# Kernel optimization log

Hardware: AMD Instinct MI355X
Metric: run time of the kernel (lower is better)

Reference implementation:

```python
import jax, jax.numpy as jnp
import numpy as np

N_EMBD = 1024
NUM_HEADS = 16
HEAD_SIZE = N_EMBD // NUM_HEADS
B, T = 2, 2048


def setup_inputs() -> dict:
    key = jax.random.key(0)
    k1, k2, k3, k4 = jax.random.split(key, 4)
    x = jax.random.normal(k1, (B, T, N_EMBD), dtype=jnp.float32)
    # torch nn.Linear weight is [out,in]; we store transposed [in,out] for x @ W
    w_qkv = jax.random.normal(k2, (N_EMBD, 3 * N_EMBD), dtype=jnp.float32) * (N_EMBD ** -0.5)
    w_proj = jax.random.normal(k3, (N_EMBD, N_EMBD), dtype=jnp.float32) * (N_EMBD ** -0.5)
    b_proj = jax.random.normal(k4, (N_EMBD,), dtype=jnp.float32) * 0.01
    return {"x": x, "w_qkv": w_qkv, "w_proj": w_proj, "b_proj": b_proj}


def reference(x, w_qkv, w_proj, b_proj):
    Bm, Tm, C = x.shape
    H, D = NUM_HEADS, HEAD_SIZE
    qkv = x @ w_qkv  # [B,T,3C]
    # einops 'b t (h d three) -> three b h t d': 'three' is the innermost factor
    qkv = qkv.reshape(Bm, Tm, H, D, 3)
    q = qkv[..., 0].transpose(0, 2, 1, 3)  # [B,H,T,D]
    k = qkv[..., 1].transpose(0, 2, 1, 3)
    v = qkv[..., 2].transpose(0, 2, 1, 3)
    scale = D ** -0.5
    attn = jnp.einsum('bhqd,bhkd->bhqk', q, k) * scale  # [B,H,T,T]
    causal_mask = jnp.triu(jnp.ones((Tm, Tm), dtype=bool), k=1)
    attn = jnp.where(causal_mask, -jnp.inf, attn)
    attn = jax.nn.softmax(attn, axis=-1)
    out = jnp.einsum('bhqk,bhkd->bhqd', attn, v)  # [B,H,T,D]
    out = out.transpose(0, 2, 1, 3).reshape(Bm, Tm, C)  # b h t d -> b t (h d)
    out = out @ w_proj + b_proj
    return out
```

## Files before the change

### kernel.cpp

```cpp
#include <hip/hip_runtime.h>
#include <hip/hip_bf16.h>
#include <math.h>

typedef __bf16 bf16x8 __attribute__((ext_vector_type(8)));
typedef __bf16 bf16x4 __attribute__((ext_vector_type(4)));
typedef float f32x4 __attribute__((ext_vector_type(4)));

#define MFMA16(A, B, C) __builtin_amdgcn_mfma_f32_16x16x32_bf16(A, B, C, 0, 0, 0)

__device__ __forceinline__ void cp16(void* lds_base, const void* g) {
  __builtin_amdgcn_global_load_lds(
      (const __attribute__((address_space(1))) void*)g,
      (__attribute__((address_space(3))) void*)lds_base, 16, 0, 0);
}

static constexpr int Bc   = 2;
static constexpr int Tc   = 2048;
static constexpr int Cc   = 1024;
static constexpr int Hc   = 16;
static constexpr int Dc   = 64;
static constexpr int Mrows = Bc * Tc;
static constexpr int N3    = 3 * Cc;

__global__ __launch_bounds__(256) void convert_x(
    const float* __restrict__ src, __bf16* __restrict__ dst, int n) {
  const int i0 = (blockIdx.x * 256 + threadIdx.x) * 8;
  if (i0 >= n) return;
  f32x4 a = *(const f32x4*)(src + i0);
  f32x4 b = *(const f32x4*)(src + i0 + 4);
  bf16x8 v;
#pragma unroll
  for (int j = 0; j < 4; ++j) { v[j] = (__bf16)a[j]; v[4 + j] = (__bf16)b[j]; }
  *(bf16x8*)(dst + i0) = v;
}

__global__ __launch_bounds__(256) void transpose_weights(
    const float* __restrict__ wqkv, const float* __restrict__ wproj,
    __bf16* __restrict__ dqkv, __bf16* __restrict__ dproj) {
  __shared__ __bf16 tile[32][33];
  const bool isproj = blockIdx.x >= 96;
  const float* src = isproj ? wproj : wqkv;
  __bf16* dst = isproj ? dproj : dqkv;
  const int N = isproj ? Cc : N3;
  const int K = Cc;
  const int n0 = (isproj ? (blockIdx.x - 96) : blockIdx.x) * 32;
  const int k0 = blockIdx.y * 32;
  const int x = threadIdx.x & 31;
  const int y = threadIdx.x >> 5;
  {
    int n = n0 + x;
    int col = n;
    if (!isproj) {
      int three = n >> 10, rem = n & 1023;
      int h = rem >> 6, d = rem & 63;
      col = h * 192 + d * 3 + three;
    }
#pragma unroll
    for (int r = 0; r < 4; ++r) {
      int k = k0 + y + r * 8;
      tile[y + r * 8][x] = (__bf16)src[(size_t)k * N + col];
    }
  }
  __syncthreads();
#pragma unroll
  for (int r = 0; r < 4; ++r) {
    int n = n0 + y + r * 8;
    dst[(size_t)n * K + k0 + x] = tile[x][y + r * 8];
  }
}

__global__ __launch_bounds__(256) void v_transpose(
    const __bf16* __restrict__ qkvp, __bf16* __restrict__ vt) {
  __shared__ __bf16 tile[32][33];
  const int t0 = blockIdx.x * 32;
  const int d0 = blockIdx.y * 32;
  const int bh = blockIdx.z;
  const int b = bh >> 4, h = bh & 15;
  const int x = threadIdx.x & 31;
  const int y = threadIdx.x >> 5;
#pragma unroll
  for (int r = 0; r < 4; ++r) {
    int t = t0 + y + r * 8;
    tile[y + r * 8][x] =
        qkvp[(size_t)(b * Tc + t) * N3 + 2 * Cc + h * 64 + d0 + x];
  }
  __syncthreads();
#pragma unroll
  for (int r = 0; r < 4; ++r) {
    int d = d0 + y + r * 8;
    vt[((size_t)bh * 64 + d) * Tc + t0 + x] = tile[x][y + r * 8];
  }
}

template <bool F32OUT>
__global__ __launch_bounds__(256) void gemm_nt(
    const __bf16* __restrict__ A, const __bf16* __restrict__ Bt,
    void* __restrict__ Cmat, const float* __restrict__ bias,
    int M, int N, int K, int ldc) {
  __shared__ __align__(16) __bf16 As[128 * 64];
  __shared__ __align__(16) __bf16 Bs[128 * 64];
  const int n0 = blockIdx.x * 128, m0 = blockIdx.y * 128;
  const int tid = threadIdx.x;
  const int wave = tid >> 6, lane = tid & 63;
  const int quad = lane >> 4, l16 = lane & 15;
  const int wm = (wave >> 1) * 64, wn = (wave & 1) * 64;
  const int srow = lane >> 3;
  const int scol = (((lane & 7) ^ (srow & 7))) * 8;

  f32x4 acc[4][4] = {};

  for (int k0 = 0; k0 < K; k0 += 64) {
    __syncthreads();
#pragma unroll
    for (int c = 0; c < 4; ++c) {
      int rowblk = c * 4 + wave;
      int row = rowblk * 8 + srow;
      cp16(&As[rowblk * 512], A + (size_t)(m0 + row) * K + k0 + scol);
      cp16(&Bs[rowblk * 512], Bt + (size_t)(n0 + row) * K + k0 + scol);
    }
    __syncthreads();
#pragma unroll
    for (int kk = 0; kk < 64; kk += 32) {
      bf16x8 af[4], bfr[4];
#pragma unroll
      for (int i = 0; i < 4; ++i) {
        int chunk = (((kk >> 3) + quad) ^ (l16 & 7)) * 8;
        af[i]  = *(const bf16x8*)(&As[(wm + i * 16 + l16) * 64 + chunk]);
        bfr[i] = *(const bf16x8*)(&Bs[(wn + i * 16 + l16) * 64 + chunk]);
      }
#pragma unroll
      for (int mi = 0; mi < 4; ++mi)
#pragma unroll
        for (int ni = 0; ni < 4; ++ni)
          acc[mi][ni] = MFMA16(af[mi], bfr[ni], acc[mi][ni]);
    }
  }

#pragma unroll
  for (int ni = 0; ni < 4; ++ni) {
    int col = n0 + wn + ni * 16 + l16;
    float bv = bias ? bias[col] : 0.0f;
#pragma unroll
    for (int mi = 0; mi < 4; ++mi)
#pragma unroll
      for (int r = 0; r < 4; ++r) {
        int row = m0 + wm + mi * 16 + quad * 4 + r;
        float v = acc[mi][ni][r] + bv;
        if (F32OUT)
          ((float*)Cmat)[(size_t)row * ldc + col] = v;
        else
          ((__bf16*)Cmat)[(size_t)row * ldc + col] = (__bf16)v;
      }
  }
}

#define LOG2E 1.44269504088896340736f
#define C2SC  (0.125f * LOG2E)
#define SH2   (16.0f * LOG2E)
static constexpr int LPK = 72;
static constexpr int LPV = 136;
static constexpr int TB  = 128;

__global__ __launch_bounds__(256) void attn_kernel(
    const __bf16* __restrict__ qkv,
    const __bf16* __restrict__ vt,
    __bf16* __restrict__ obuf) {
  __shared__ __align__(16) __bf16 Ks[TB * LPK];
  __shared__ __align__(16) __bf16 Vs[64 * LPV];
  __shared__ __align__(16) __bf16 plds[4][2][16 * LPK];

  const int bh = blockIdx.x;
  const int torder = blockIdx.y;
  const int qt = (torder < 8) ? torder : (23 - torder);
  const int q0 = qt * 128;
  const int b = bh >> 4, hh = bh & 15;
  const int tid = threadIdx.x;
  const int wave = tid >> 6, lane = tid & 63;
  const int quad = lane >> 4, l16 = lane & 15;
  const int qb = q0 + wave * 32;
  const int kblocks = q0 + 128;

  const __bf16* qbase = qkv + (size_t)(b * Tc) * N3 + hh * 64;
  const __bf16* kbase = qbase + Cc;
  const __bf16* vtb = vt + (size_t)bh * 64 * Tc;

  const int krow = tid >> 1;
  const int kcol = (tid & 1) * 32;
  const int vrow = tid >> 2;
  const int vcol = (tid & 3) * 32;

  bf16x8 bQ[2][2];
#pragma unroll
  for (int hf = 0; hf < 2; ++hf) {
    const __bf16* qr = qbase + (size_t)(qb + hf * 16 + l16) * N3;
    bQ[hf][0] = *(const bf16x8*)(qr + quad * 8);
    bQ[hf][1] = *(const bf16x8*)(qr + 32 + quad * 8);
  }

  f32x4 accO[2][4] = {};
  float l_part[2] = {0.0f, 0.0f};

  bf16x8 kp[4], vp[4];
  {
    const __bf16* kr = kbase + (size_t)krow * N3 + kcol;
    const __bf16* vr = vtb + (size_t)vrow * Tc + vcol;
#pragma unroll
    for (int j = 0; j < 4; ++j) {
      kp[j] = *(const bf16x8*)(kr + j * 8);
      vp[j] = *(const bf16x8*)(vr + j * 8);
    }
  }

  for (int kc = 0; kc < kblocks; kc += TB) {
    __syncthreads();
#pragma unroll
    for (int j = 0; j < 4; ++j) {
      *(bf16x8*)(&Ks[krow * LPK + kcol + j * 8]) = kp[j];
      *(bf16x8*)(&Vs[vrow * LPV + vcol + j * 8]) = vp[j];
    }
    if (kc + TB < kblocks) {
      const __bf16* kr = kbase + (size_t)(kc + TB + krow) * N3 + kcol;
      const __bf16* vr = vtb + (size_t)vrow * Tc + kc + TB + vcol;
#pragma unroll
      for (int j = 0; j < 4; ++j) {
        kp[j] = *(const bf16x8*)(kr + j * 8);
        vp[j] = *(const bf16x8*)(vr + j * 8);
      }
    }
    __syncthreads();

#pragma unroll
    for (int sub = 0; sub < 2; ++sub) {
      const int kc2 = kc + sub * 64;
      if (kc2 >= qb + 32) continue;

      f32x4 st[2][4];
#pragma unroll
      for (int kt = 0; kt < 4; ++kt) {
        const int trow = sub * 64 + kt * 16 + l16;
        bf16x8 kf0 = *(const bf16x8*)(&Ks[trow * LPK + quad * 8]);
        bf16x8 kf1 = *(const bf16x8*)(&Ks[trow * LPK + 32 + quad * 8]);
#pragma unroll
        for (int hf = 0; hf < 2; ++hf) {
          f32x4 a = {};
          a = MFMA16(kf0, bQ[hf][0], a);
          a = MFMA16(kf1, bQ[hf][1], a);
          st[hf][kt] = a;
        }
      }
      if (kc2 + 64 > qb) {
#pragma unroll
        for (int hf = 0; hf < 2; ++hf) {
          int qcol = qb + hf * 16 + l16;
#pragma unroll
          for (int kt = 0; kt < 4; ++kt)
#pragma unroll
            for (int r = 0; r < 4; ++r) {
              int t = kc2 + kt * 16 + quad * 4 + r;
              if (t > qcol) st[hf][kt][r] = -INFINITY;
            }
        }
      }
#pragma unroll
      for (int hf = 0; hf < 2; ++hf)
#pragma unroll
        for (int kt = 0; kt < 4; ++kt)
#pragma unroll
          for (int r = 0; r < 4; ++r) {
            float p = __builtin_amdgcn_exp2f(fmaf(st[hf][kt][r], C2SC, -SH2));
            st[hf][kt][r] = p;
            l_part[hf] += p;
          }
#pragma unroll
      for (int hf = 0; hf < 2; ++hf)
#pragma unroll
        for (int kt = 0; kt < 4; ++kt) {
          bf16x4 pv;
#pragma unroll
          for (int r = 0; r < 4; ++r) pv[r] = (__bf16)st[hf][kt][r];
          *(bf16x4*)(&plds[wave][hf][l16 * LPK + kt * 16 + quad * 4]) = pv;
        }
      __threadfence_block();
      bf16x8 bP[2][2];
#pragma unroll
      for (int hf = 0; hf < 2; ++hf) {
        bP[hf][0] = *(const bf16x8*)(&plds[wave][hf][l16 * LPK + quad * 8]);
        bP[hf][1] = *(const bf16x8*)(&plds[wave][hf][l16 * LPK + 32 + quad * 8]);
      }
#pragma unroll
      for (int dt = 0; dt < 4; ++dt) {
        const int drow = (dt * 16 + l16) * LPV + sub * 64;
        bf16x8 vf0 = *(const bf16x8*)(&Vs[drow + quad * 8]);
        bf16x8 vf1 = *(const bf16x8*)(&Vs[drow + 32 + quad * 8]);
#pragma unroll
        for (int hf = 0; hf < 2; ++hf) {
          accO[hf][dt] = MFMA16(vf0, bP[hf][0], accO[hf][dt]);
          accO[hf][dt] = MFMA16(vf1, bP[hf][1], accO[hf][dt]);
        }
      }
    }
  }

#pragma unroll
  for (int hf = 0; hf < 2; ++hf) {
    float l_i = l_part[hf];
    l_i += __shfl_xor(l_i, 16);
    l_i += __shfl_xor(l_i, 32);
    float inv = 1.0f / l_i;
    __bf16* orow = obuf + (size_t)(b * Tc + qb + hf * 16 + l16) * Cc + hh * 64;
#pragma unroll
    for (int dt = 0; dt < 4; ++dt) {
      bf16x4 ov;
#pragma unroll
      for (int r = 0; r < 4; ++r) ov[r] = (__bf16)(accO[hf][dt][r] * inv);
      *(bf16x4*)(orow + dt * 16 + quad * 4) = ov;
    }
  }
}

extern "C" void kernel_launch(void* const* d_in, const int* in_sizes, int n_in,
                              void* d_out, int out_size, void* d_ws, size_t ws_size,
                              hipStream_t stream) {
  const float* x      = (const float*)d_in[0];
  const float* w_qkv  = (const float*)d_in[1];
  const float* w_proj = (const float*)d_in[2];
  const float* b_proj = (const float*)d_in[3];

  bool f32out = true;
  {
    size_t out_bytes = 0;
    if (hipMemPtrGetInfo(d_out, &out_bytes) == hipSuccess && out_bytes != 0)
      f32out = out_bytes >= (size_t)out_size * 4;
  }

  __bf16* xb     = (__bf16*)d_ws;
  __bf16* wqkvT  = xb + (size_t)Mrows * Cc;
  __bf16* wprojT = wqkvT + (size_t)N3 * Cc;
  __bf16* qkvp   = wprojT + (size_t)Cc * Cc;
  __bf16* vt     = qkvp + (size_t)Mrows * N3;
  __bf16* obuf   = vt + (size_t)Bc * Hc * Dc * Tc;

  convert_x<<<(Mrows * Cc) / (256 * 8), 256, 0, stream>>>(x, xb, Mrows * Cc);
  transpose_weights<<<dim3(128, 32), 256, 0, stream>>>(
      w_qkv, w_proj, wqkvT, wprojT);
  gemm_nt<false><<<dim3(N3 / 128, Mrows / 128), 256, 0, stream>>>(
      xb, wqkvT, qkvp, nullptr, Mrows, N3, Cc, N3);
  v_transpose<<<dim3(Tc / 32, 2, Bc * Hc), 256, 0, stream>>>(qkvp, vt);
  attn_kernel<<<dim3(Bc * Hc, 16), 256, 0, stream>>>(qkvp, vt, obuf);
  if (f32out) {
    gemm_nt<true><<<dim3(Cc / 128, Mrows / 128), 256, 0, stream>>>(
        obuf, wprojT, d_out, b_proj, Mrows, Cc, Cc, Cc);
  } else {
    gemm_nt<false><<<dim3(Cc / 128, Mrows / 128), 256, 0, stream>>>(
        obuf, wprojT, d_out, b_proj, Mrows, Cc, Cc, Cc);
  }
}
```

Baseline: 182.1 us.

## Split attention block across 8 waves with 16 query rows each

The attention kernel now runs 512 threads (8 waves) per block, and each wave handles 16 query rows instead of 32. K/V tile loading is spread across twice as many threads, and per-wave P scratch and accumulators are halved. The aim is more waves per CU for latency hiding and lower register pressure. In exchange, each K/V fragment read from LDS feeds half as many MFMAs, and block-wide syncs now cover more waves.

```diff
diff --git a/kernel.cpp b/kernel.cpp
--- a/kernel.cpp
+++ b/kernel.cpp
@@ -161,13 +161,13 @@
 static constexpr int LPV = 136;
 static constexpr int TB  = 128;
 
-__global__ __launch_bounds__(256) void attn_kernel(
+__global__ __launch_bounds__(512, 4) void attn_kernel(
     const __bf16* __restrict__ qkv,
     const __bf16* __restrict__ vt,
     __bf16* __restrict__ obuf) {
   __shared__ __align__(16) __bf16 Ks[TB * LPK];
   __shared__ __align__(16) __bf16 Vs[64 * LPV];
-  __shared__ __align__(16) __bf16 plds[4][2][16 * LPK];
+  __shared__ __align__(16) __bf16 plds[8][16 * LPK];
 
   const int bh = blockIdx.x;
   const int torder = blockIdx.y;
@@ -177,35 +177,34 @@
   const int tid = threadIdx.x;
   const int wave = tid >> 6, lane = tid & 63;
   const int quad = lane >> 4, l16 = lane & 15;
-  const int qb = q0 + wave * 32;
+  const int qb = q0 + wave * 16;
   const int kblocks = q0 + 128;
 
   const __bf16* qbase = qkv + (size_t)(b * Tc) * N3 + hh * 64;
   const __bf16* kbase = qbase + Cc;
   const __bf16* vtb = vt + (size_t)bh * 64 * Tc;
 
-  const int krow = tid >> 1;
-  const int kcol = (tid & 1) * 32;
-  const int vrow = tid >> 2;
-  const int vcol = (tid & 3) * 32;
-
-  bf16x8 bQ[2][2];
-#pragma unroll
-  for (int hf = 0; hf < 2; ++hf) {
-    const __bf16* qr = qbase + (size_t)(qb + hf * 16 + l16) * N3;
-    bQ[hf][0] = *(const bf16x8*)(qr + quad * 8);
-    bQ[hf][1] = *(const bf16x8*)(qr + 32 + quad * 8);
-  }
-
-  f32x4 accO[2][4] = {};
-  float l_part[2] = {0.0f, 0.0f};
-
-  bf16x8 kp[4], vp[4];
+  const int krow = tid >> 2;
+  const int kcol = (tid & 3) * 16;
+  const int vrow = tid >> 3;
+  const int vcol = (tid & 7) * 16;
+
+  bf16x8 bQ[2];
+  {
+    const __bf16* qr = qbase + (size_t)(qb + l16) * N3;
+    bQ[0] = *(const bf16x8*)(qr + quad * 8);
+    bQ[1] = *(const bf16x8*)(qr + 32 + quad * 8);
+  }
+
+  f32x4 accO[4] = {};
+  float l_part = 0.0f;
+
+  bf16x8 kp[2], vp[2];
   {
     const __bf16* kr = kbase + (size_t)krow * N3 + kcol;
     const __bf16* vr = vtb + (size_t)vrow * Tc + vcol;
 #pragma unroll
-    for (int j = 0; j < 4; ++j) {
+    for (int j = 0; j < 2; ++j) {
       kp[j] = *(const bf16x8*)(kr + j * 8);
       vp[j] = *(const bf16x8*)(vr + j * 8);
     }
@@ -214,7 +213,7 @@
   for (int kc = 0; kc < kblocks; kc += TB) {
     __syncthreads();
 #pragma unroll
-    for (int j = 0; j < 4; ++j) {
+    for (int j = 0; j < 2; ++j) {
       *(bf16x8*)(&Ks[krow * LPK + kcol + j * 8]) = kp[j];
       *(bf16x8*)(&Vs[vrow * LPV + vcol + j * 8]) = vp[j];
     }
@@ -222,7 +221,7 @@
       const __bf16* kr = kbase + (size_t)(kc + TB + krow) * N3 + kcol;
       const __bf16* vr = vtb + (size_t)vrow * Tc + kc + TB + vcol;
 #pragma unroll
-      for (int j = 0; j < 4; ++j) {
+      for (int j = 0; j < 2; ++j) {
         kp[j] = *(const bf16x8*)(kr + j * 8);
         vp[j] = *(const bf16x8*)(vr + j * 8);
       }
@@ -232,87 +231,70 @@
 #pragma unroll
     for (int sub = 0; sub < 2; ++sub) {
       const int kc2 = kc + sub * 64;
-      if (kc2 >= qb + 32) continue;
-
-      f32x4 st[2][4];
+      if (kc2 >= qb + 16) continue;
+
+      f32x4 st[4];
 #pragma unroll
       for (int kt = 0; kt < 4; ++kt) {
         const int trow = sub * 64 + kt * 16 + l16;
         bf16x8 kf0 = *(const bf16x8*)(&Ks[trow * LPK + quad * 8]);
         bf16x8 kf1 = *(const bf16x8*)(&Ks[trow * LPK + 32 + quad * 8]);
-#pragma unroll
-        for (int hf = 0; hf < 2; ++hf) {
-          f32x4 a = {};
-          a = MFMA16(kf0, bQ[hf][0], a);
-          a = MFMA16(kf1, bQ[hf][1], a);
-          st[hf][kt] = a;
+        f32x4 a = {};
+        a = MFMA16(kf0, bQ[0], a);
+        a = MFMA16(kf1, bQ[1], a);
+        st[kt] = a;
+      }
+      if (kc2 + 64 > qb) {
+        int qcol = qb + l16;
+#pragma unroll
+        for (int kt = 0; kt < 4; ++kt)
+#pragma unroll
+          for (int r = 0; r < 4; ++r) {
+            int t = kc2 + kt * 16 + quad * 4 + r;
+            if (t > qcol) st[kt][r] = -INFINITY;
+          }
+      }
+#pragma unroll
+      for (int kt = 0; kt < 4; ++kt)
+#pragma unroll
+        for (int r = 0; r < 4; ++r) {
+          float p = __builtin_amdgcn_exp2f(fmaf(st[kt][r], C2SC, -SH2));
+          st[kt][r] = p;
+          l_part += p;
         }
-      }
-      if (kc2 + 64 > qb) {
-#pragma unroll
-        for (int hf = 0; hf < 2; ++hf) {
-          int qcol = qb + hf * 16 + l16;
-#pragma unroll
-          for (int kt = 0; kt < 4; ++kt)
-#pragma unroll
-            for (int r = 0; r < 4; ++r) {
-              int t = kc2 + kt * 16 + quad * 4 + r;
-              if (t > qcol) st[hf][kt][r] = -INFINITY;
-            }
-        }
-      }
-#pragma unroll
-      for (int hf = 0; hf < 2; ++hf)
-#pragma unroll
-        for (int kt = 0; kt < 4; ++kt)
-#pragma unroll
-          for (int r = 0; r < 4; ++r) {
-            float p = __builtin_amdgcn_exp2f(fmaf(st[hf][kt][r], C2SC, -SH2));
-            st[hf][kt][r] = p;
-            l_part[hf] += p;
-          }
-#pragma unroll
-      for (int hf = 0; hf < 2; ++hf)
-#pragma unroll
-        for (int kt = 0; kt < 4; ++kt) {
-          bf16x4 pv;
-#pragma unroll
-          for (int r = 0; r < 4; ++r) pv[r] = (__bf16)st[hf][kt][r];
-          *(bf16x4*)(&plds[wave][hf][l16 * LPK + kt * 16 + quad * 4]) = pv;
-        }
+#pragma unroll
+      for (int kt = 0; kt < 4; ++kt) {
+        bf16x4 pv;
+#pragma unroll
+        for (int r = 0; r < 4; ++r) pv[r] = (__bf16)st[kt][r];
+        *(bf16x4*)(&plds[wave][l16 * LPK + kt * 16 + quad * 4]) = pv;
+      }
       __threadfence_block();
-      bf16x8 bP[2][2];
-#pragma unroll
-      for (int hf = 0; hf < 2; ++hf) {
-        bP[hf][0] = *(const bf16x8*)(&plds[wave][hf][l16 * LPK + quad * 8]);
-        bP[hf][1] = *(const bf16x8*)(&plds[wave][hf][l16 * LPK + 32 + quad * 8]);
-      }
+      bf16x8 bP[2];
+      bP[0] = *(const bf16x8*)(&plds[wave][l16 * LPK + quad * 8]);
+      bP[1] = *(const bf16x8*)(&plds[wave][l16 * LPK + 32 + quad * 8]);
 #pragma unroll
       for (int dt = 0; dt < 4; ++dt) {
         const int drow = (dt * 16 + l16) * LPV + sub * 64;
         bf16x8 vf0 = *(const bf16x8*)(&Vs[drow + quad * 8]);
         bf16x8 vf1 = *(const bf16x8*)(&Vs[drow + 32 + quad * 8]);
-#pragma unroll
-        for (int hf = 0; hf < 2; ++hf) {
-          accO[hf][dt] = MFMA16(vf0, bP[hf][0], accO[hf][dt]);
-          accO[hf][dt] = MFMA16(vf1, bP[hf][1], accO[hf][dt]);
-        }
-      }
-    }
-  }
-
-#pragma unroll
-  for (int hf = 0; hf < 2; ++hf) {
-    float l_i = l_part[hf];
+        accO[dt] = MFMA16(vf0, bP[0], accO[dt]);
+        accO[dt] = MFMA16(vf1, bP[1], accO[dt]);
+      }
+    }
+  }
+
+  {
+    float l_i = l_part;
     l_i += __shfl_xor(l_i, 16);
     l_i += __shfl_xor(l_i, 32);
     float inv = 1.0f / l_i;
-    __bf16* orow = obuf + (size_t)(b * Tc + qb + hf * 16 + l16) * Cc + hh * 64;
+    __bf16* orow = obuf + (size_t)(b * Tc + qb + l16) * Cc + hh * 64;
 #pragma unroll
     for (int dt = 0; dt < 4; ++dt) {
       bf16x4 ov;
 #pragma unroll
-      for (int r = 0; r < 4; ++r) ov[r] = (__bf16)(accO[hf][dt][r] * inv);
+      for (int r = 0; r < 4; ++r) ov[r] = (__bf16)(accO[dt][r] * inv);
       *(bf16x4*)(orow + dt * 16 + quad * 4) = ov;
     }
   }
@@ -346,7 +328,7 @@
   gemm_nt<false><<<dim3(N3 / 128, Mrows / 128), 256, 0, stream>>>(
       xb, wqkvT, qkvp, nullptr, Mrows, N3, Cc, N3);
   v_transpose<<<dim3(Tc / 32, 2, Bc * Hc), 256, 0, stream>>>(qkvp, vt);
-  attn_kernel<<<dim3(Bc * Hc, 16), 256, 0, stream>>>(qkvp, vt, obuf);
+  attn_kernel<<<dim3(Bc * Hc, 16), 512, 0, stream>>>(qkvp, vt, obuf);
   if (f32out) {
     gemm_nt<true><<<dim3(Cc / 128, Mrows / 128), 256, 0, stream>>>(
         obuf, wprojT, d_out, b_proj, Mrows, Cc, Cc, Cc);
```

Result: faster. 175.3 us, median of 2 (-3.7%).

## Use single-wave attention blocks reading K/V directly from global memory

Applied to the files above, without the earlier changes.

The attention kernel shrinks from 4-wave blocks of 128 queries that stage K and V tiles in LDS to single-wave blocks of 32 queries that load K and V fragments straight from global memory (relying on L2/L1 caching). This removes the __syncthreads barriers and LDS staging, and raises the block count from 512 to 2048 for better load balance across CUs. In exchange, K/V tiles are no longer shared across waves, so global/cache traffic rises about fourfold, and loads are not prefetched ahead of compute.

```diff
diff --git a/kernel.cpp b/kernel.cpp
--- a/kernel.cpp
+++ b/kernel.cpp
@@ -158,41 +158,29 @@
 #define C2SC  (0.125f * LOG2E)
 #define SH2   (16.0f * LOG2E)
 static constexpr int LPK = 72;
-static constexpr int LPV = 136;
-static constexpr int TB  = 128;
-
-__global__ __launch_bounds__(256) void attn_kernel(
+
+__global__ __launch_bounds__(64, 2) void attn_kernel(
     const __bf16* __restrict__ qkv,
     const __bf16* __restrict__ vt,
     __bf16* __restrict__ obuf) {
-  __shared__ __align__(16) __bf16 Ks[TB * LPK];
-  __shared__ __align__(16) __bf16 Vs[64 * LPV];
-  __shared__ __align__(16) __bf16 plds[4][2][16 * LPK];
+  __shared__ __align__(16) __bf16 plds[2][16 * LPK];
 
   const int bh = blockIdx.x;
-  const int torder = blockIdx.y;
-  const int qt = (torder < 8) ? torder : (23 - torder);
-  const int q0 = qt * 128;
+  const int y = blockIdx.y;
+  const int qt = (y < 32) ? y : 95 - y;
+  const int q0 = qt * 32;
   const int b = bh >> 4, hh = bh & 15;
-  const int tid = threadIdx.x;
-  const int wave = tid >> 6, lane = tid & 63;
+  const int lane = threadIdx.x;
   const int quad = lane >> 4, l16 = lane & 15;
-  const int qb = q0 + wave * 32;
-  const int kblocks = q0 + 128;
 
   const __bf16* qbase = qkv + (size_t)(b * Tc) * N3 + hh * 64;
   const __bf16* kbase = qbase + Cc;
   const __bf16* vtb = vt + (size_t)bh * 64 * Tc;
 
-  const int krow = tid >> 1;
-  const int kcol = (tid & 1) * 32;
-  const int vrow = tid >> 2;
-  const int vcol = (tid & 3) * 32;
-
   bf16x8 bQ[2][2];
 #pragma unroll
   for (int hf = 0; hf < 2; ++hf) {
-    const __bf16* qr = qbase + (size_t)(qb + hf * 16 + l16) * N3;
+    const __bf16* qr = qbase + (size_t)(q0 + hf * 16 + l16) * N3;
     bQ[hf][0] = *(const bf16x8*)(qr + quad * 8);
     bQ[hf][1] = *(const bf16x8*)(qr + 32 + quad * 8);
   }
@@ -200,103 +188,69 @@
   f32x4 accO[2][4] = {};
   float l_part[2] = {0.0f, 0.0f};
 
-  bf16x8 kp[4], vp[4];
-  {
-    const __bf16* kr = kbase + (size_t)krow * N3 + kcol;
-    const __bf16* vr = vtb + (size_t)vrow * Tc + vcol;
-#pragma unroll
-    for (int j = 0; j < 4; ++j) {
-      kp[j] = *(const bf16x8*)(kr + j * 8);
-      vp[j] = *(const bf16x8*)(vr + j * 8);
-    }
-  }
-
-  for (int kc = 0; kc < kblocks; kc += TB) {
-    __syncthreads();
-#pragma unroll
-    for (int j = 0; j < 4; ++j) {
-      *(bf16x8*)(&Ks[krow * LPK + kcol + j * 8]) = kp[j];
-      *(bf16x8*)(&Vs[vrow * LPV + vcol + j * 8]) = vp[j];
-    }
-    if (kc + TB < kblocks) {
-      const __bf16* kr = kbase + (size_t)(kc + TB + krow) * N3 + kcol;
-      const __bf16* vr = vtb + (size_t)vrow * Tc + kc + TB + vcol;
-#pragma unroll
-      for (int j = 0; j < 4; ++j) {
-        kp[j] = *(const bf16x8*)(kr + j * 8);
-        vp[j] = *(const bf16x8*)(vr + j * 8);
-      }
-    }
-    __syncthreads();
-
-#pragma unroll
-    for (int sub = 0; sub < 2; ++sub) {
-      const int kc2 = kc + sub * 64;
-      if (kc2 >= qb + 32) continue;
-
-      f32x4 st[2][4];
+  for (int kc = 0; kc <= q0 + 31; kc += 64) {
+    f32x4 st[2][4];
+#pragma unroll
+    for (int kt = 0; kt < 4; ++kt) {
+      const __bf16* kr = kbase + (size_t)(kc + kt * 16 + l16) * N3;
+      bf16x8 kf0 = *(const bf16x8*)(kr + quad * 8);
+      bf16x8 kf1 = *(const bf16x8*)(kr + 32 + quad * 8);
+#pragma unroll
+      for (int hf = 0; hf < 2; ++hf) {
+        f32x4 a = {};
+        a = MFMA16(kf0, bQ[hf][0], a);
+        a = MFMA16(kf1, bQ[hf][1], a);
+        st[hf][kt] = a;
+      }
+    }
+    if (kc + 64 > q0) {
+#pragma unroll
+      for (int hf = 0; hf < 2; ++hf) {
+        int qcol = q0 + hf * 16 + l16;
+#pragma unroll
+        for (int kt = 0; kt < 4; ++kt)
+#pragma unroll
+          for (int r = 0; r < 4; ++r) {
+            int t = kc + kt * 16 + quad * 4 + r;
+            if (t > qcol) st[hf][kt][r] = -INFINITY;
+          }
+      }
+    }
+#pragma unroll
+    for (int hf = 0; hf < 2; ++hf)
+#pragma unroll
+      for (int kt = 0; kt < 4; ++kt)
+#pragma unroll
+        for (int r = 0; r < 4; ++r) {
+          float p = __builtin_amdgcn_exp2f(fmaf(st[hf][kt][r], C2SC, -SH2));
+          st[hf][kt][r] = p;
+          l_part[hf] += p;
+        }
+#pragma unroll
+    for (int hf = 0; hf < 2; ++hf)
 #pragma unroll
       for (int kt = 0; kt < 4; ++kt) {
-        const int trow = sub * 64 + kt * 16 + l16;
-        bf16x8 kf0 = *(const bf16x8*)(&Ks[trow * LPK + quad * 8]);
-        bf16x8 kf1 = *(const bf16x8*)(&Ks[trow * LPK + 32 + quad * 8]);
-#pragma unroll
-        for (int hf = 0; hf < 2; ++hf) {
-          f32x4 a = {};
-          a = MFMA16(kf0, bQ[hf][0], a);
-          a = MFMA16(kf1, bQ[hf][1], a);
-          st[hf][kt] = a;
-        }
-      }
-      if (kc2 + 64 > qb) {
-#pragma unroll
-        for (int hf = 0; hf < 2; ++hf) {
-          int qcol = qb + hf * 16 + l16;
-#pragma unroll
-          for (int kt = 0; kt < 4; ++kt)
-#pragma unroll
-            for (int r = 0; r < 4; ++r) {
-              int t = kc2 + kt * 16 + quad * 4 + r;
-              if (t > qcol) st[hf][kt][r] = -INFINITY;
-            }
-        }
-      }
-#pragma unroll
-      for (int hf = 0; hf < 2; ++hf)
-#pragma unroll
-        for (int kt = 0; kt < 4; ++kt)
-#pragma unroll
-          for (int r = 0; r < 4; ++r) {
-            float p = __builtin_amdgcn_exp2f(fmaf(st[hf][kt][r], C2SC, -SH2));
-            st[hf][kt][r] = p;
-            l_part[hf] += p;
-          }
-#pragma unroll
-      for (int hf = 0; hf < 2; ++hf)
-#pragma unroll
-        for (int kt = 0; kt < 4; ++kt) {
-          bf16x4 pv;
-#pragma unroll
-          for (int r = 0; r < 4; ++r) pv[r] = (__bf16)st[hf][kt][r];
-          *(bf16x4*)(&plds[wave][hf][l16 * LPK + kt * 16 + quad * 4]) = pv;
-        }
-      __threadfence_block();
-      bf16x8 bP[2][2];
+        bf16x4 pv;
+#pragma unroll
+        for (int r = 0; r < 4; ++r) pv[r] = (__bf16)st[hf][kt][r];
+        *(bf16x4*)(&plds[hf][l16 * LPK + kt * 16 + quad * 4]) = pv;
+      }
+    __threadfence_block();
+    bf16x8 bP[2][2];
+#pragma unroll
+    for (int hf = 0; hf < 2; ++hf) {
+      bP[hf][0] = *(const bf16x8*)(&plds[hf][l16 * LPK + quad * 8]);
+      bP[hf][1] = *(const bf16x8*)(&plds[hf][l16 * LPK + 32 + quad * 8]);
+    }
+#pragma unroll
+    for (int dt = 0; dt < 4; ++dt) {
+      const __bf16* vr = vtb + (size_t)(dt * 16 + l16) * Tc + kc;
+      bf16x8 vf0 = *(const bf16x8*)(vr + quad * 8);
+      bf16x8 vf1 = *(const bf16x8*)(vr + 32 + quad * 8);
 #pragma unroll
       for (int hf = 0; hf < 2; ++hf) {
-        bP[hf][0] = *(const bf16x8*)(&plds[wave][hf][l16 * LPK + quad * 8]);
-        bP[hf][1] = *(const bf16x8*)(&plds[wave][hf][l16 * LPK + 32 + quad * 8]);
-      }
-#pragma unroll
-      for (int dt = 0; dt < 4; ++dt) {
-        const int drow = (dt * 16 + l16) * LPV + sub * 64;
-        bf16x8 vf0 = *(const bf16x8*)(&Vs[drow + quad * 8]);
-        bf16x8 vf1 = *(const bf16x8*)(&Vs[drow + 32 + quad * 8]);
-#pragma unroll
-        for (int hf = 0; hf < 2; ++hf) {
-          accO[hf][dt] = MFMA16(vf0, bP[hf][0], accO[hf][dt]);
-          accO[hf][dt] = MFMA16(vf1, bP[hf][1], accO[hf][dt]);
-        }
+        accO[hf][dt] = MFMA16(vf0, bP[hf][0], accO[hf][dt]);
+        accO[hf][dt] = MFMA16(vf1, bP[hf][1], accO[hf][dt]);
       }
     }
   }
@@ -307,7 +261,7 @@
     l_i += __shfl_xor(l_i, 16);
     l_i += __shfl_xor(l_i, 32);
     float inv = 1.0f / l_i;
-    __bf16* orow = obuf + (size_t)(b * Tc + qb + hf * 16 + l16) * Cc + hh * 64;
+    __bf16* orow = obuf + (size_t)(b * Tc + q0 + hf * 16 + l16) * Cc + hh * 64;
 #pragma unroll
     for (int dt = 0; dt < 4; ++dt) {
       bf16x4 ov;
@@ -346,7 +300,7 @@
   gemm_nt<false><<<dim3(N3 / 128, Mrows / 128), 256, 0, stream>>>(
       xb, wqkvT, qkvp, nullptr, Mrows, N3, Cc, N3);
   v_transpose<<<dim3(Tc / 32, 2, Bc * Hc), 256, 0, stream>>>(qkvp, vt);
-  attn_kernel<<<dim3(Bc * Hc, 16), 256, 0, stream>>>(qkvp, vt, obuf);
+  attn_kernel<<<dim3(Bc * Hc, 64), 64, 0, stream>>>(qkvp, vt, obuf);
   if (f32out) {
     gemm_nt<true><<<dim3(Cc / 128, Mrows / 128), 256, 0, stream>>>(
         obuf, wprojT, d_out, b_proj, Mrows, Cc, Cc, Cc);
```

After: 241.3 us. 1.33x slower.

## Pair causal q-tiles per block and split key halves across wave groups

Applied to the files above, without the earlier changes.

Attention blocks now use 8 waves and process two complementary q-tiles (i and 15-i) sequentially, so causal work per block is equal. Within a key block, wave groups handle separate 64-key halves for the same queries, and partial outputs and row sums are merged through shared memory at the end. MFMA sections get raised wave priority. This aims to fix load imbalance and raise per-block parallelism, at the cost of extra syncs, a merge step and more LDS per block.

```diff
diff --git a/kernel.cpp b/kernel.cpp
--- a/kernel.cpp
+++ b/kernel.cpp
@@ -160,160 +160,205 @@
 static constexpr int LPK = 72;
 static constexpr int LPV = 136;
 static constexpr int TB  = 128;
-
-__global__ __launch_bounds__(256) void attn_kernel(
+static constexpr int KS_ELE = TB * LPK;
+static constexpr int VS_ELE = 64 * LPV;
+static constexpr int PL_STR = 16 * LPK;
+static constexpr int PL_ELE = 8 * 2 * PL_STR;
+
+__global__ __launch_bounds__(512, 2) void attn_kernel(
     const __bf16* __restrict__ qkv,
     const __bf16* __restrict__ vt,
     __bf16* __restrict__ obuf) {
-  __shared__ __align__(16) __bf16 Ks[TB * LPK];
-  __shared__ __align__(16) __bf16 Vs[64 * LPV];
-  __shared__ __align__(16) __bf16 plds[4][2][16 * LPK];
+  __shared__ __align__(16) __bf16 smem[KS_ELE + VS_ELE + PL_ELE];
+  __bf16* const Ks = smem;
+  __bf16* const Vs = smem + KS_ELE;
+  __bf16* const plds = smem + KS_ELE + VS_ELE;
+  float* const fmerge = (float*)smem;
 
   const int bh = blockIdx.x;
-  const int torder = blockIdx.y;
-  const int qt = (torder < 8) ? torder : (23 - torder);
-  const int q0 = qt * 128;
+  const int pairidx = blockIdx.y;
   const int b = bh >> 4, hh = bh & 15;
   const int tid = threadIdx.x;
   const int wave = tid >> 6, lane = tid & 63;
   const int quad = lane >> 4, l16 = lane & 15;
-  const int qb = q0 + wave * 32;
-  const int kblocks = q0 + 128;
+  const int s  = wave & 3;
+  const int pr = wave >> 2;
 
   const __bf16* qbase = qkv + (size_t)(b * Tc) * N3 + hh * 64;
   const __bf16* kbase = qbase + Cc;
   const __bf16* vtb = vt + (size_t)bh * 64 * Tc;
 
-  const int krow = tid >> 1;
-  const int kcol = (tid & 1) * 32;
-  const int vrow = tid >> 2;
-  const int vcol = (tid & 3) * 32;
-
-  bf16x8 bQ[2][2];
-#pragma unroll
-  for (int hf = 0; hf < 2; ++hf) {
-    const __bf16* qr = qbase + (size_t)(qb + hf * 16 + l16) * N3;
-    bQ[hf][0] = *(const bf16x8*)(qr + quad * 8);
-    bQ[hf][1] = *(const bf16x8*)(qr + 32 + quad * 8);
-  }
-
-  f32x4 accO[2][4] = {};
-  float l_part[2] = {0.0f, 0.0f};
-
-  bf16x8 kp[4], vp[4];
-  {
-    const __bf16* kr = kbase + (size_t)krow * N3 + kcol;
-    const __bf16* vr = vtb + (size_t)vrow * Tc + vcol;
-#pragma unroll
-    for (int j = 0; j < 4; ++j) {
-      kp[j] = *(const bf16x8*)(kr + j * 8);
-      vp[j] = *(const bf16x8*)(vr + j * 8);
-    }
-  }
-
-  for (int kc = 0; kc < kblocks; kc += TB) {
-    __syncthreads();
-#pragma unroll
-    for (int j = 0; j < 4; ++j) {
-      *(bf16x8*)(&Ks[krow * LPK + kcol + j * 8]) = kp[j];
-      *(bf16x8*)(&Vs[vrow * LPV + vcol + j * 8]) = vp[j];
-    }
-    if (kc + TB < kblocks) {
-      const __bf16* kr = kbase + (size_t)(kc + TB + krow) * N3 + kcol;
-      const __bf16* vr = vtb + (size_t)vrow * Tc + kc + TB + vcol;
-#pragma unroll
-      for (int j = 0; j < 4; ++j) {
+  const int krow = tid >> 2;
+  const int kcol = (tid & 3) * 16;
+  const int vrow = tid >> 3;
+  const int vcol = (tid & 7) * 16;
+
+#pragma unroll
+  for (int pi = 0; pi < 2; ++pi) {
+    const int qt = pi ? (15 - pairidx) : pairidx;
+    const int q0 = qt * 128;
+    const int qb = q0 + s * 32;
+    const int kblocks = q0 + 128;
+
+    bf16x8 bQ[2][2];
+#pragma unroll
+    for (int hf = 0; hf < 2; ++hf) {
+      const __bf16* qr = qbase + (size_t)(qb + hf * 16 + l16) * N3;
+      bQ[hf][0] = *(const bf16x8*)(qr + quad * 8);
+      bQ[hf][1] = *(const bf16x8*)(qr + 32 + quad * 8);
+    }
+
+    f32x4 accO[2][4] = {};
+    float l_part[2] = {0.0f, 0.0f};
+
+    bf16x8 kp[2], vp[2];
+    {
+      const __bf16* kr = kbase + (size_t)krow * N3 + kcol;
+      const __bf16* vr = vtb + (size_t)vrow * Tc + vcol;
+#pragma unroll
+      for (int j = 0; j < 2; ++j) {
         kp[j] = *(const bf16x8*)(kr + j * 8);
         vp[j] = *(const bf16x8*)(vr + j * 8);
       }
     }
+
+    for (int kc = 0; kc < kblocks; kc += TB) {
+      __syncthreads();
+#pragma unroll
+      for (int j = 0; j < 2; ++j) {
+        *(bf16x8*)(&Ks[krow * LPK + kcol + j * 8]) = kp[j];
+        *(bf16x8*)(&Vs[vrow * LPV + vcol + j * 8]) = vp[j];
+      }
+      if (kc + TB < kblocks) {
+        const __bf16* kr = kbase + (size_t)(kc + TB + krow) * N3 + kcol;
+        const __bf16* vr = vtb + (size_t)vrow * Tc + kc + TB + vcol;
+#pragma unroll
+        for (int j = 0; j < 2; ++j) {
+          kp[j] = *(const bf16x8*)(kr + j * 8);
+          vp[j] = *(const bf16x8*)(vr + j * 8);
+        }
+      }
+      __syncthreads();
+
+      const int kc2 = kc + pr * 64;
+      if (kc2 < qb + 32) {
+        f32x4 st[2][4];
+        __builtin_amdgcn_s_setprio(1);
+#pragma unroll
+        for (int kt = 0; kt < 4; ++kt) {
+          const int trow = pr * 64 + kt * 16 + l16;
+          bf16x8 kf0 = *(const bf16x8*)(&Ks[trow * LPK + quad * 8]);
+          bf16x8 kf1 = *(const bf16x8*)(&Ks[trow * LPK + 32 + quad * 8]);
+#pragma unroll
+          for (int hf = 0; hf < 2; ++hf) {
+            f32x4 a = {};
+            a = MFMA16(kf0, bQ[hf][0], a);
+            a = MFMA16(kf1, bQ[hf][1], a);
+            st[hf][kt] = a;
+          }
+        }
+        __builtin_amdgcn_s_setprio(0);
+        if (kc2 + 64 > qb) {
+#pragma unroll
+          for (int hf = 0; hf < 2; ++hf) {
+            int qcol = qb + hf * 16 + l16;
+#pragma unroll
+            for (int kt = 0; kt < 4; ++kt)
+#pragma unroll
+              for (int r = 0; r < 4; ++r) {
+                int t = kc2 + kt * 16 + quad * 4 + r;
+                if (t > qcol) st[hf][kt][r] = -INFINITY;
+              }
+          }
+        }
+#pragma unroll
+        for (int hf = 0; hf < 2; ++hf)
+#pragma unroll
+          for (int kt = 0; kt < 4; ++kt)
+#pragma unroll
+            for (int r = 0; r < 4; ++r) {
+              float p = __builtin_amdgcn_exp2f(fmaf(st[hf][kt][r], C2SC, -SH2));
+              st[hf][kt][r] = p;
+              l_part[hf] += p;
+            }
+#pragma unroll
+        for (int hf = 0; hf < 2; ++hf)
+#pragma unroll
+          for (int kt = 0; kt < 4; ++kt) {
+            bf16x4 pv;
+#pragma unroll
+            for (int r = 0; r < 4; ++r) pv[r] = (__bf16)st[hf][kt][r];
+            *(bf16x4*)(&plds[(wave * 2 + hf) * PL_STR + l16 * LPK +
+                             kt * 16 + quad * 4]) = pv;
+          }
+        __threadfence_block();
+        bf16x8 bP[2][2];
+#pragma unroll
+        for (int hf = 0; hf < 2; ++hf) {
+          const __bf16* pb = &plds[(wave * 2 + hf) * PL_STR + l16 * LPK];
+          bP[hf][0] = *(const bf16x8*)(pb + quad * 8);
+          bP[hf][1] = *(const bf16x8*)(pb + 32 + quad * 8);
+        }
+        __builtin_amdgcn_s_setprio(1);
+#pragma unroll
+        for (int dt = 0; dt < 4; ++dt) {
+          const int drow = (dt * 16 + l16) * LPV + pr * 64;
+          bf16x8 vf0 = *(const bf16x8*)(&Vs[drow + quad * 8]);
+          bf16x8 vf1 = *(const bf16x8*)(&Vs[drow + 32 + quad * 8]);
+#pragma unroll
+          for (int hf = 0; hf < 2; ++hf) {
+            accO[hf][dt] = MFMA16(vf0, bP[hf][0], accO[hf][dt]);
+            accO[hf][dt] = MFMA16(vf1, bP[hf][1], accO[hf][dt]);
+          }
+        }
+        __builtin_amdgcn_s_setprio(0);
+      }
+    }
+
     __syncthreads();
-
-#pragma unroll
-    for (int sub = 0; sub < 2; ++sub) {
-      const int kc2 = kc + sub * 64;
-      if (kc2 >= qb + 32) continue;
-
-      f32x4 st[2][4];
-#pragma unroll
-      for (int kt = 0; kt < 4; ++kt) {
-        const int trow = sub * 64 + kt * 16 + l16;
-        bf16x8 kf0 = *(const bf16x8*)(&Ks[trow * LPK + quad * 8]);
-        bf16x8 kf1 = *(const bf16x8*)(&Ks[trow * LPK + 32 + quad * 8]);
-#pragma unroll
-        for (int hf = 0; hf < 2; ++hf) {
-          f32x4 a = {};
-          a = MFMA16(kf0, bQ[hf][0], a);
-          a = MFMA16(kf1, bQ[hf][1], a);
-          st[hf][kt] = a;
-        }
-      }
-      if (kc2 + 64 > qb) {
-#pragma unroll
-        for (int hf = 0; hf < 2; ++hf) {
-          int qcol = qb + hf * 16 + l16;
-#pragma unroll
-          for (int kt = 0; kt < 4; ++kt)
-#pragma unroll
-            for (int r = 0; r < 4; ++r) {
-              int t = kc2 + kt * 16 + quad * 4 + r;
-              if (t > qcol) st[hf][kt][r] = -INFINITY;
-            }
-        }
-      }
+    if (pr == 1) {
+      float* fa = fmerge + (size_t)(s * 64 + lane) * 32;
 #pragma unroll
       for (int hf = 0; hf < 2; ++hf)
 #pragma unroll
-        for (int kt = 0; kt < 4; ++kt)
-#pragma unroll
-          for (int r = 0; r < 4; ++r) {
-            float p = __builtin_amdgcn_exp2f(fmaf(st[hf][kt][r], C2SC, -SH2));
-            st[hf][kt][r] = p;
-            l_part[hf] += p;
-          }
+        for (int dt = 0; dt < 4; ++dt)
+#pragma unroll
+          for (int r = 0; r < 4; ++r)
+            fa[(hf * 4 + dt) * 4 + r] = accO[hf][dt][r];
+      float* fl = fmerge + 8192 + (s * 64 + lane) * 2;
+      fl[0] = l_part[0];
+      fl[1] = l_part[1];
+    }
+    __syncthreads();
+    if (pr == 0) {
+      float* fa = fmerge + (size_t)(s * 64 + lane) * 32;
 #pragma unroll
       for (int hf = 0; hf < 2; ++hf)
 #pragma unroll
-        for (int kt = 0; kt < 4; ++kt) {
-          bf16x4 pv;
-#pragma unroll
-          for (int r = 0; r < 4; ++r) pv[r] = (__bf16)st[hf][kt][r];
-          *(bf16x4*)(&plds[wave][hf][l16 * LPK + kt * 16 + quad * 4]) = pv;
-        }
-      __threadfence_block();
-      bf16x8 bP[2][2];
+        for (int dt = 0; dt < 4; ++dt)
+#pragma unroll
+          for (int r = 0; r < 4; ++r)
+            accO[hf][dt][r] += fa[(hf * 4 + dt) * 4 + r];
+      float* fl = fmerge + 8192 + (s * 64 + lane) * 2;
+      l_part[0] += fl[0];
+      l_part[1] += fl[1];
+
 #pragma unroll
       for (int hf = 0; hf < 2; ++hf) {
-        bP[hf][0] = *(const bf16x8*)(&plds[wave][hf][l16 * LPK + quad * 8]);
-        bP[hf][1] = *(const bf16x8*)(&plds[wave][hf][l16 * LPK + 32 + quad * 8]);
-      }
-#pragma unroll
-      for (int dt = 0; dt < 4; ++dt) {
-        const int drow = (dt * 16 + l16) * LPV + sub * 64;
-        bf16x8 vf0 = *(const bf16x8*)(&Vs[drow + quad * 8]);
-        bf16x8 vf1 = *(const bf16x8*)(&Vs[drow + 32 + quad * 8]);
-#pragma unroll
-        for (int hf = 0; hf < 2; ++hf) {
-          accO[hf][dt] = MFMA16(vf0, bP[hf][0], accO[hf][dt]);
-          accO[hf][dt] = MFMA16(vf1, bP[hf][1], accO[hf][dt]);
-        }
-      }
-    }
-  }
-
-#pragma unroll
-  for (int hf = 0; hf < 2; ++hf) {
-    float l_i = l_part[hf];
-    l_i += __shfl_xor(l_i, 16);
-    l_i += __shfl_xor(l_i, 32);
-    float inv = 1.0f / l_i;
-    __bf16* orow = obuf + (size_t)(b * Tc + qb + hf * 16 + l16) * Cc + hh * 64;
-#pragma unroll
-    for (int dt = 0; dt < 4; ++dt) {
-      bf16x4 ov;
-#pragma unroll
-      for (int r = 0; r < 4; ++r) ov[r] = (__bf16)(accO[hf][dt][r] * inv);
-      *(bf16x4*)(orow + dt * 16 + quad * 4) = ov;
+        float l_i = l_part[hf];
+        l_i += __shfl_xor(l_i, 16);
+        l_i += __shfl_xor(l_i, 32);
+        float inv = 1.0f / l_i;
+        __bf16* orow =
+            obuf + (size_t)(b * Tc + qb + hf * 16 + l16) * Cc + hh * 64;
+#pragma unroll
+        for (int dt = 0; dt < 4; ++dt) {
+          bf16x4 ov;
+#pragma unroll
+          for (int r = 0; r < 4; ++r) ov[r] = (__bf16)(accO[hf][dt][r] * inv);
+          *(bf16x4*)(orow + dt * 16 + quad * 4) = ov;
+        }
+      }
     }
   }
 }
@@ -346,7 +391,7 @@
   gemm_nt<false><<<dim3(N3 / 128, Mrows / 128), 256, 0, stream>>>(
       xb, wqkvT, qkvp, nullptr, Mrows, N3, Cc, N3);
   v_transpose<<<dim3(Tc / 32, 2, Bc * Hc), 256, 0, stream>>>(qkvp, vt);
-  attn_kernel<<<dim3(Bc * Hc, 16), 256, 0, stream>>>(qkvp, vt, obuf);
+  attn_kernel<<<dim3(Bc * Hc, 8), 512, 0, stream>>>(qkvp, vt, obuf);
   if (f32out) {
     gemm_nt<true><<<dim3(Cc / 128, Mrows / 128), 256, 0, stream>>>(
         obuf, wprojT, d_out, b_proj, Mrows, Cc, Cc, Cc);
```

Result: faster. 176.9 us (-2.9%).
